# Performance work log

Measured on AMD Instinct MI355X. Metric: run time of the kernel, lower is better.

The kernel has to match this reference:

```python
import jax, jax.numpy as jnp
import numpy as np

DIM = 384
D_STATE = 16


def setup_inputs() -> dict:
    key = jax.random.key(0)
    ks = jax.random.split(key, 8)
    B, C, H, W = 4, DIM, 64, 64
    x = jax.random.normal(ks[0], (B, C, H, W), dtype=jnp.float32)
    P = 2 * DIM + 2 * D_STATE  # proj output width
    W_proj = jax.random.normal(ks[1], (P, DIM), dtype=jnp.float32) * 0.02
    b_proj = jnp.zeros((P,), dtype=jnp.float32)
    # A_log = log(uniform(0,1) + 1e-4) as in torch init
    A_log = jnp.log(jax.random.uniform(ks[2], (DIM, D_STATE), dtype=jnp.float32) + 1e-4)
    D = jnp.ones((DIM,), dtype=jnp.float32)
    dt_bias = jnp.zeros((DIM,), dtype=jnp.float32)
    W_out = jax.random.normal(ks[3], (DIM, DIM), dtype=jnp.float32) * 0.02
    b_out = jnp.zeros((DIM,), dtype=jnp.float32)
    return {"x": x, "W_proj": W_proj, "b_proj": b_proj, "A_log": A_log,
            "D": D, "dt_bias": dt_bias, "W_out": W_out, "b_out": b_out}


def _selective_scan(x_in, delta, A, Bm, Cm, D):
    # x_in, delta: (B, L, dim); Bm, Cm: (B, L, n); A: (dim, n); D: (dim,)
    Bsz, L, dim = x_in.shape
    n = A.shape[1]

    def step(h, inp):
        d_t, x_t, b_t, c_t = inp  # (B,dim),(B,dim),(B,n),(B,n)
        # h: (B, dim, n)
        h = jnp.exp(d_t[..., None] * A) * h + (d_t * x_t)[..., None] * b_t[:, None, :]
        y_t = jnp.einsum('bdn,bn->bd', h, c_t)
        return h, y_t

    h0 = jnp.zeros((Bsz, dim, n), dtype=x_in.dtype)
    xs = (jnp.swapaxes(delta, 0, 1), jnp.swapaxes(x_in, 0, 1),
          jnp.swapaxes(Bm, 0, 1), jnp.swapaxes(Cm, 0, 1))
    _, ys = jax.lax.scan(step, h0, xs)  # ys: (L, B, dim)
    y = jnp.swapaxes(ys, 0, 1)  # (B, L, dim)
    return y + x_in * D


def reference(x, W_proj, b_proj, A_log, D, dt_bias, W_out, b_out):
    B, C, H, W = x.shape
    L = H * W
    seq = x.reshape(B, C, L).transpose(0, 2, 1)  # (B, L, C)
    proj = seq @ W_proj.T + b_proj  # (B, L, 2*dim + 2*n)
    x_in = proj[..., :DIM]
    delta = proj[..., DIM:2 * DIM]
    Bm = proj[..., 2 * DIM:2 * DIM + D_STATE]
    Cm = proj[..., 2 * DIM + D_STATE:]
    A = -jnp.exp(A_log)  # (dim, n)
    delta = jax.nn.softplus(delta + dt_bias)  # delta_bias + delta_softplus
    y = _selective_scan(x_in, delta, A, Bm, Cm, D)  # (B, L, dim)
    out = y @ W_out.T + b_out  # (B, L, dim)
    return out.transpose(0, 2, 1).reshape(B, C, H, W)
```

## Files before the change

kernel.cpp:

```cpp
#include <hip/hip_runtime.h>
#include <cstdint>
#include <cstddef>

#define DIMC 384
#define DST  16
#define LLEN 4096
#define NB   4
#define PDIM 800
#define NCH  64
#define CL   64
#define KDIM 384

typedef __attribute__((ext_vector_type(8))) short bf16x8;
typedef __attribute__((ext_vector_type(4))) float f32x4;

#define GLOAD16(g, l) __builtin_amdgcn_global_load_lds( \
    (const __attribute__((address_space(1))) uint32_t*)(g), \
    (__attribute__((address_space(3))) uint32_t*)(l), 16, 0, 0)

__device__ __forceinline__ float softplus_f(float v) {
    if (v > 20.f) return v;
    return logf(1.f + __expf(v));
}

__device__ __forceinline__ ushort f2bf(float x) {
    uint32_t u = __float_as_uint(x);
    uint32_t r = (u + 0x7FFFu + ((u >> 16) & 1u)) >> 16;
    return (ushort)r;
}

__global__ __launch_bounds__(256)
void cast_bf(const float* __restrict__ in, ushort* __restrict__ out,
             int n_src, int n_tot)
{
    int i = (blockIdx.x * 256 + threadIdx.x) * 4;
    if (i >= n_tot) return;
    if (i < n_src) {
        float4 v = *(const float4*)(in + i);
        ushort4 s; s.x = f2bf(v.x); s.y = f2bf(v.y); s.z = f2bf(v.z); s.w = f2bf(v.w);
        *(ushort4*)(out + i) = s;
    } else {
        ushort4 s; s.x = 0; s.y = 0; s.z = 0; s.w = 0;
        *(ushort4*)(out + i) = s;
    }
}

__global__ __launch_bounds__(256)
void transpose_cast(const float* __restrict__ in, ushort* __restrict__ out)
{
    __shared__ float t[64][65];
    const int tid = threadIdx.x;
    const int b  = blockIdx.z;
    const int c0 = blockIdx.y * 64;
    const int l0 = blockIdx.x * 64;
    const float* ip = in + ((size_t)b * DIMC + c0) * LLEN + l0;
    #pragma unroll
    for (int r = 0; r < 4; ++r) {
        int cl = (tid >> 4) + r * 16;
        int l4 = (tid & 15) * 4;
        float4 v = *(const float4*)(ip + (size_t)cl * LLEN + l4);
        t[cl][l4 + 0] = v.x; t[cl][l4 + 1] = v.y;
        t[cl][l4 + 2] = v.z; t[cl][l4 + 3] = v.w;
    }
    __syncthreads();
    ushort* op = out + ((size_t)b * LLEN + l0) * DIMC + c0;
    #pragma unroll
    for (int r = 0; r < 4; ++r) {
        int ll = (tid >> 4) + r * 16;
        int c4 = (tid & 15) * 4;
        ushort4 s;
        s.x = f2bf(t[c4 + 0][ll]); s.y = f2bf(t[c4 + 1][ll]);
        s.z = f2bf(t[c4 + 2][ll]); s.w = f2bf(t[c4 + 3][ll]);
        *(ushort4*)(op + (size_t)ll * DIMC + c4) = s;
    }
}

template<int EPI>
__global__ __launch_bounds__(256)
void mfma_gemm(const ushort* __restrict__ Abf, const ushort* __restrict__ Wbf,
               const float* __restrict__ bias, const float* __restrict__ dt_bias,
               float* __restrict__ o_x, float* __restrict__ o_dt,
               float* __restrict__ o_Bm, float* __restrict__ o_Cm,
               float* __restrict__ o_out)
{
    __shared__ ushort Alds[128 * 32];
    __shared__ ushort Blds[64 * 32];

    const int tid = threadIdx.x;
    const int m0  = blockIdx.x * 128;
    const int n0  = blockIdx.y * 64;
    const int w   = tid >> 6;
    const int ln  = tid & 63;
    const int wm  = w * 32;
    const int fr  = ln & 15;
    const int fg  = ln >> 4;

    const int srow = tid >> 2;
    const int sg   = tid & 3;

    const ushort* Ag = Abf + (size_t)m0 * KDIM;
    const ushort* Bg = Wbf + (size_t)n0 * KDIM;

    f32x4 acc[2][4];
    #pragma unroll
    for (int i = 0; i < 2; ++i)
        #pragma unroll
        for (int j = 0; j < 4; ++j)
            acc[i][j] = (f32x4){0.f, 0.f, 0.f, 0.f};

    for (int k0 = 0; k0 < KDIM; k0 += 32) {
        if (k0) __syncthreads();
        {
            int a0 = sg ^ ((srow >> 1) & 3);
            GLOAD16(Ag + (size_t)srow * KDIM + k0 + a0 * 8, &Alds[tid * 8]);
            int r1 = srow + 64;
            int a1 = sg ^ ((r1 >> 1) & 3);
            GLOAD16(Ag + (size_t)r1 * KDIM + k0 + a1 * 8, &Alds[2048 + tid * 8]);
            GLOAD16(Bg + (size_t)srow * KDIM + k0 + a0 * 8, &Blds[tid * 8]);
        }
        __syncthreads();
        bf16x8 af[2], bfv[4];
        #pragma unroll
        for (int i = 0; i < 2; ++i) {
            int r = wm + i * 16 + fr;
            af[i] = *(const bf16x8*)&Alds[r * 32 + ((fg ^ ((r >> 1) & 3)) << 3)];
        }
        #pragma unroll
        for (int j = 0; j < 4; ++j) {
            int r = j * 16 + fr;
            bfv[j] = *(const bf16x8*)&Blds[r * 32 + ((fg ^ ((r >> 1) & 3)) << 3)];
        }
        #pragma unroll
        for (int i = 0; i < 2; ++i)
            #pragma unroll
            for (int j = 0; j < 4; ++j)
                acc[i][j] = __builtin_amdgcn_mfma_f32_16x16x32_bf16(af[i], bfv[j], acc[i][j], 0, 0, 0);
    }

    const int b   = m0 / LLEN;
    const int ml0 = m0 - b * LLEN;
    #pragma unroll
    for (int j = 0; j < 4; ++j) {
        const int n = n0 + j * 16 + fr;
        #pragma unroll
        for (int i = 0; i < 2; ++i) {
            const int l = ml0 + wm + i * 16 + fg * 4;
            f32x4 v = acc[i][j];
            if (EPI == 0) {
                if (n < DIMC) {
                    const float bb = bias[n];
                    float4 st; st.x = v[0] + bb; st.y = v[1] + bb; st.z = v[2] + bb; st.w = v[3] + bb;
                    *(float4*)(o_x + ((size_t)b * DIMC + n) * LLEN + l) = st;
                } else if (n < 2 * DIMC) {
                    const int d = n - DIMC;
                    const float bb = bias[n] + dt_bias[d];
                    float4 st;
                    st.x = softplus_f(v[0] + bb); st.y = softplus_f(v[1] + bb);
                    st.z = softplus_f(v[2] + bb); st.w = softplus_f(v[3] + bb);
                    *(float4*)(o_dt + ((size_t)b * DIMC + d) * LLEN + l) = st;
                } else if (n < 2 * DIMC + DST) {
                    const int s = n - 2 * DIMC;
                    const float bb = bias[n];
                    #pragma unroll
                    for (int r = 0; r < 4; ++r)
                        o_Bm[((size_t)b * LLEN + l + r) * DST + s] = v[r] + bb;
                } else if (n < PDIM) {
                    const int s = n - 2 * DIMC - DST;
                    const float bb = bias[n];
                    #pragma unroll
                    for (int r = 0; r < 4; ++r)
                        o_Cm[((size_t)b * LLEN + l + r) * DST + s] = v[r] + bb;
                }
            } else {
                const float bb = bias[n];
                float4 st; st.x = v[0] + bb; st.y = v[1] + bb; st.z = v[2] + bb; st.w = v[3] + bb;
                *(float4*)(o_out + ((size_t)b * DIMC + n) * LLEN + l) = st;
            }
        }
    }
}

__global__ __launch_bounds__(256)
void scan_part1(const float* __restrict__ dt_t, const float* __restrict__ x_t,
                const float* __restrict__ Bm, const float* __restrict__ A_log,
                float* __restrict__ Pc, float* __restrict__ Qc)
{
    const int tid = threadIdx.x;
    const int n   = tid & 15;
    const int g   = blockIdx.x * 16 + (tid >> 4);
    const int bd  = g >> 6;
    const int chk = g & (NCH - 1);
    const int b   = bd / DIMC;
    const int d   = bd - b * DIMC;

    const float Aval = -__expf(A_log[d * DST + n]);
    const float* dtp = dt_t + (size_t)bd * LLEN + chk * CL;
    const float* xp  = x_t  + (size_t)bd * LLEN + chk * CL;
    const float* Bp  = Bm + ((size_t)b * LLEN + chk * CL) * DST + n;

    float P = 1.f, q = 0.f;
    for (int t0 = 0; t0 < CL; t0 += 4) {
        float4 dt4 = *(const float4*)(dtp + t0);
        float4 x4  = *(const float4*)(xp + t0);
        float bv[4];
        #pragma unroll
        for (int j = 0; j < 4; ++j) bv[j] = Bp[(size_t)(t0 + j) * DST];
        float dts[4] = {dt4.x, dt4.y, dt4.z, dt4.w};
        float xs[4]  = {x4.x, x4.y, x4.z, x4.w};
        #pragma unroll
        for (int j = 0; j < 4; ++j) {
            float a = __expf(dts[j] * Aval);
            P *= a;
            q = fmaf(a, q, dts[j] * xs[j] * bv[j]);
        }
    }
    Pc[(size_t)g * DST + n] = P;
    Qc[(size_t)g * DST + n] = q;
}

__global__ __launch_bounds__(256)
void scan_carry(const float* __restrict__ Pc, const float* __restrict__ Qc,
                float* __restrict__ Hin)
{
    const int idx = blockIdx.x * 256 + threadIdx.x;
    const int bd  = idx >> 4;
    const int n   = idx & 15;
    float h = 0.f;
    for (int chk = 0; chk < NCH; ++chk) {
        size_t o = ((size_t)bd * NCH + chk) * DST + n;
        Hin[o] = h;
        h = fmaf(Pc[o], h, Qc[o]);
    }
}

__global__ __launch_bounds__(256)
void scan_part3(const float* __restrict__ dt_t, const float* __restrict__ x_t,
                const float* __restrict__ Bm, const float* __restrict__ Cm,
                const float* __restrict__ A_log, const float* __restrict__ Dv,
                const float* __restrict__ Hin, float* __restrict__ y_t)
{
    const int tid = threadIdx.x;
    const int n   = tid & 15;
    const int g   = blockIdx.x * 16 + (tid >> 4);
    const int bd  = g >> 6;
    const int chk = g & (NCH - 1);
    const int b   = bd / DIMC;
    const int d   = bd - b * DIMC;

    const float Aval = -__expf(A_log[d * DST + n]);
    const float Dd   = Dv[d];
    const float* dtp = dt_t + (size_t)bd * LLEN + chk * CL;
    const float* xp  = x_t  + (size_t)bd * LLEN + chk * CL;
    const float* Bp  = Bm + ((size_t)b * LLEN + chk * CL) * DST + n;
    const float* Cp  = Cm + ((size_t)b * LLEN + chk * CL) * DST + n;
    float*       yp  = y_t + (size_t)bd * LLEN + chk * CL;

    float h = Hin[(size_t)g * DST + n];
    for (int t0 = 0; t0 < CL; t0 += 4) {
        float4 dt4 = *(const float4*)(dtp + t0);
        float4 x4  = *(const float4*)(xp + t0);
        float bv[4], cv[4];
        #pragma unroll
        for (int j = 0; j < 4; ++j) {
            bv[j] = Bp[(size_t)(t0 + j) * DST];
            cv[j] = Cp[(size_t)(t0 + j) * DST];
        }
        float dts[4] = {dt4.x, dt4.y, dt4.z, dt4.w};
        float xs[4]  = {x4.x, x4.y, x4.z, x4.w};
        float ys[4];
        #pragma unroll
        for (int j = 0; j < 4; ++j) {
            float a = __expf(dts[j] * Aval);
            h = fmaf(a, h, dts[j] * xs[j] * bv[j]);
            float p = h * cv[j];
            p += __shfl_xor(p, 1);
            p += __shfl_xor(p, 2);
            p += __shfl_xor(p, 4);
            p += __shfl_xor(p, 8);
            ys[j] = fmaf(xs[j], Dd, p);
        }
        if (n == 0) {
            float4 st; st.x = ys[0]; st.y = ys[1]; st.z = ys[2]; st.w = ys[3];
            *(float4*)(yp + t0) = st;
        }
    }
}

extern "C" void kernel_launch(void* const* d_in, const int* in_sizes, int n_in,
                              void* d_out, int out_size, void* d_ws, size_t ws_size,
                              hipStream_t stream)
{
    const float* x      = (const float*)d_in[0];
    const float* W_proj = (const float*)d_in[1];
    const float* b_proj = (const float*)d_in[2];
    const float* A_log  = (const float*)d_in[3];
    const float* Dv     = (const float*)d_in[4];
    const float* dt_b   = (const float*)d_in[5];
    const float* W_out  = (const float*)d_in[6];
    const float* b_out  = (const float*)d_in[7];
    float* out = (float*)d_out;
    float* ws  = (float*)d_ws;

    const size_t szBD = (size_t)NB * DIMC * LLEN;
    const size_t szBC = (size_t)NB * LLEN * DST;
    const size_t szPQ = (size_t)NB * DIMC * NCH * DST;
    float* x_t  = ws;
    float* dt_t = x_t + szBD;
    float* Bmw  = dt_t + szBD;
    float* Cmw  = Bmw + szBC;
    float* y_t  = Cmw + szBC;
    float* Pc   = y_t + szBD;
    float* Qc   = Pc + szPQ;
    float* Hin  = Qc + szPQ;
    ushort* x_bfT = (ushort*)(Hin + szPQ);
    ushort* y_bfT = x_bfT + szBD;
    ushort* Wp_bf = y_bfT + szBD;
    ushort* Wo_bf = Wp_bf + (size_t)832 * KDIM;

    cast_bf<<<(832 * KDIM) / 1024, 256, 0, stream>>>(W_proj, Wp_bf,
                                                     PDIM * KDIM, 832 * KDIM);
    cast_bf<<<(DIMC * KDIM) / 1024, 256, 0, stream>>>(W_out, Wo_bf,
                                                      DIMC * KDIM, DIMC * KDIM);
    dim3 tg(LLEN / 64, DIMC / 64, NB);
    transpose_cast<<<tg, 256, 0, stream>>>(x, x_bfT);

    dim3 g1((NB * LLEN) / 128, (PDIM + 63) / 64);
    mfma_gemm<0><<<g1, 256, 0, stream>>>(x_bfT, Wp_bf, b_proj, dt_b,
                                         x_t, dt_t, Bmw, Cmw, nullptr);

    const int ngroups = NB * DIMC * NCH;
    scan_part1<<<ngroups / 16, 256, 0, stream>>>(dt_t, x_t, Bmw, A_log, Pc, Qc);
    scan_carry<<<(NB * DIMC * DST) / 256, 256, 0, stream>>>(Pc, Qc, Hin);
    scan_part3<<<ngroups / 16, 256, 0, stream>>>(dt_t, x_t, Bmw, Cmw,
                                                 A_log, Dv, Hin, y_t);

    transpose_cast<<<tg, 256, 0, stream>>>(y_t, y_bfT);

    dim3 g2((NB * LLEN) / 128, DIMC / 64);
    mfma_gemm<1><<<g2, 256, 0, stream>>>(y_bfT, Wo_bf, b_out, nullptr,
                                         nullptr, nullptr, nullptr, nullptr,
                                         out);
}
```

Measured before the change: 248.7 us.

## Restructure chunked scan to thread-per-channel and fuse bf16 transpose into scan output

The scan kernels now give each thread one (batch, channel) with all 16 state lanes held in registers, instead of one lane per thread. B and C for the chunk are staged in shared memory, which removes the per-step shuffle reduction. scan_part3 writes its output directly as transposed bf16, so the separate transpose_cast pass and the fp32 y buffer are gone. The chunk length is halved to 32 and the number of chunks doubled, which keeps enough blocks in flight (512 blocks of 384 threads) at the cost of heavier register use and a longer serial carry pass.

```diff
diff --git a/kernel.cpp b/kernel.cpp
--- a/kernel.cpp
+++ b/kernel.cpp
@@ -7,8 +7,8 @@
 #define LLEN 4096
 #define NB   4
 #define PDIM 800
-#define NCH  64
-#define CL   64
+#define NCH  128
+#define CL   32
 #define KDIM 384
 
 typedef __attribute__((ext_vector_type(8))) short bf16x8;
@@ -180,42 +180,60 @@
     }
 }
 
-__global__ __launch_bounds__(256)
+__global__ __launch_bounds__(384)
 void scan_part1(const float* __restrict__ dt_t, const float* __restrict__ x_t,
                 const float* __restrict__ Bm, const float* __restrict__ A_log,
                 float* __restrict__ Pc, float* __restrict__ Qc)
 {
-    const int tid = threadIdx.x;
-    const int n   = tid & 15;
-    const int g   = blockIdx.x * 16 + (tid >> 4);
-    const int bd  = g >> 6;
-    const int chk = g & (NCH - 1);
-    const int b   = bd / DIMC;
-    const int d   = bd - b * DIMC;
-
-    const float Aval = -__expf(A_log[d * DST + n]);
-    const float* dtp = dt_t + (size_t)bd * LLEN + chk * CL;
-    const float* xp  = x_t  + (size_t)bd * LLEN + chk * CL;
-    const float* Bp  = Bm + ((size_t)b * LLEN + chk * CL) * DST + n;
-
-    float P = 1.f, q = 0.f;
+    __shared__ float Bs[CL][DST];
+    const int d   = threadIdx.x;
+    const int b   = blockIdx.x >> 7;
+    const int chk = blockIdx.x & (NCH - 1);
+    const int l0  = chk * CL;
+
+    if (d < (CL * DST) / 4)
+        ((float4*)&Bs[0][0])[d] =
+            ((const float4*)(Bm + ((size_t)b * LLEN + l0) * DST))[d];
+
+    float Av[DST];
+    #pragma unroll
+    for (int r = 0; r < 4; ++r) {
+        float4 v = *(const float4*)(A_log + d * DST + r * 4);
+        Av[r*4+0] = -__expf(v.x); Av[r*4+1] = -__expf(v.y);
+        Av[r*4+2] = -__expf(v.z); Av[r*4+3] = -__expf(v.w);
+    }
+    __syncthreads();
+
+    const float* dtp = dt_t + ((size_t)b * DIMC + d) * LLEN + l0;
+    const float* xp  = x_t  + ((size_t)b * DIMC + d) * LLEN + l0;
+
+    float P[DST], q[DST];
+    #pragma unroll
+    for (int n = 0; n < DST; ++n) { P[n] = 1.f; q[n] = 0.f; }
+
     for (int t0 = 0; t0 < CL; t0 += 4) {
         float4 dt4 = *(const float4*)(dtp + t0);
         float4 x4  = *(const float4*)(xp + t0);
-        float bv[4];
-        #pragma unroll
-        for (int j = 0; j < 4; ++j) bv[j] = Bp[(size_t)(t0 + j) * DST];
         float dts[4] = {dt4.x, dt4.y, dt4.z, dt4.w};
         float xs[4]  = {x4.x, x4.y, x4.z, x4.w};
         #pragma unroll
         for (int j = 0; j < 4; ++j) {
-            float a = __expf(dts[j] * Aval);
-            P *= a;
-            q = fmaf(a, q, dts[j] * xs[j] * bv[j]);
-        }
-    }
-    Pc[(size_t)g * DST + n] = P;
-    Qc[(size_t)g * DST + n] = q;
+            const float dt  = dts[j];
+            const float dtx = dt * xs[j];
+            #pragma unroll
+            for (int n = 0; n < DST; ++n) {
+                float a = __expf(dt * Av[n]);
+                P[n] *= a;
+                q[n] = fmaf(a, q[n], dtx * Bs[t0 + j][n]);
+            }
+        }
+    }
+    const size_t o = (((size_t)b * NCH + chk) * DIMC + d) * DST;
+    #pragma unroll
+    for (int r = 0; r < 4; ++r) {
+        *(float4*)(Pc + o + r * 4) = *(float4*)&P[r * 4];
+        *(float4*)(Qc + o + r * 4) = *(float4*)&q[r * 4];
+    }
 }
 
 __global__ __launch_bounds__(256)
@@ -225,63 +243,74 @@
     const int idx = blockIdx.x * 256 + threadIdx.x;
     const int bd  = idx >> 4;
     const int n   = idx & 15;
+    const int b   = bd / DIMC;
+    const int d   = bd - b * DIMC;
     float h = 0.f;
     for (int chk = 0; chk < NCH; ++chk) {
-        size_t o = ((size_t)bd * NCH + chk) * DST + n;
+        const size_t o = (((size_t)b * NCH + chk) * DIMC + d) * DST + n;
         Hin[o] = h;
         h = fmaf(Pc[o], h, Qc[o]);
     }
 }
 
-__global__ __launch_bounds__(256)
+__global__ __launch_bounds__(384)
 void scan_part3(const float* __restrict__ dt_t, const float* __restrict__ x_t,
                 const float* __restrict__ Bm, const float* __restrict__ Cm,
                 const float* __restrict__ A_log, const float* __restrict__ Dv,
-                const float* __restrict__ Hin, float* __restrict__ y_t)
-{
-    const int tid = threadIdx.x;
-    const int n   = tid & 15;
-    const int g   = blockIdx.x * 16 + (tid >> 4);
-    const int bd  = g >> 6;
-    const int chk = g & (NCH - 1);
-    const int b   = bd / DIMC;
-    const int d   = bd - b * DIMC;
-
-    const float Aval = -__expf(A_log[d * DST + n]);
-    const float Dd   = Dv[d];
-    const float* dtp = dt_t + (size_t)bd * LLEN + chk * CL;
-    const float* xp  = x_t  + (size_t)bd * LLEN + chk * CL;
-    const float* Bp  = Bm + ((size_t)b * LLEN + chk * CL) * DST + n;
-    const float* Cp  = Cm + ((size_t)b * LLEN + chk * CL) * DST + n;
-    float*       yp  = y_t + (size_t)bd * LLEN + chk * CL;
-
-    float h = Hin[(size_t)g * DST + n];
+                const float* __restrict__ Hin, ushort* __restrict__ y_bfT)
+{
+    __shared__ float Bs[CL][DST];
+    __shared__ float Cs[CL][DST];
+    const int d   = threadIdx.x;
+    const int b   = blockIdx.x >> 7;
+    const int chk = blockIdx.x & (NCH - 1);
+    const int l0  = chk * CL;
+
+    if (d < 128)
+        ((float4*)&Bs[0][0])[d] =
+            ((const float4*)(Bm + ((size_t)b * LLEN + l0) * DST))[d];
+    else if (d < 256)
+        ((float4*)&Cs[0][0])[d - 128] =
+            ((const float4*)(Cm + ((size_t)b * LLEN + l0) * DST))[d - 128];
+
+    float Av[DST];
+    #pragma unroll
+    for (int r = 0; r < 4; ++r) {
+        float4 v = *(const float4*)(A_log + d * DST + r * 4);
+        Av[r*4+0] = -__expf(v.x); Av[r*4+1] = -__expf(v.y);
+        Av[r*4+2] = -__expf(v.z); Av[r*4+3] = -__expf(v.w);
+    }
+    const float Dd = Dv[d];
+    __syncthreads();
+
+    float h[DST];
+    const size_t ho = (((size_t)b * NCH + chk) * DIMC + d) * DST;
+    #pragma unroll
+    for (int r = 0; r < 4; ++r)
+        *(float4*)&h[r * 4] = *(const float4*)(Hin + ho + r * 4);
+
+    const float* dtp = dt_t + ((size_t)b * DIMC + d) * LLEN + l0;
+    const float* xp  = x_t  + ((size_t)b * DIMC + d) * LLEN + l0;
+    ushort* yp = y_bfT + ((size_t)b * LLEN + l0) * DIMC + d;
+
     for (int t0 = 0; t0 < CL; t0 += 4) {
         float4 dt4 = *(const float4*)(dtp + t0);
         float4 x4  = *(const float4*)(xp + t0);
-        float bv[4], cv[4];
-        #pragma unroll
-        for (int j = 0; j < 4; ++j) {
-            bv[j] = Bp[(size_t)(t0 + j) * DST];
-            cv[j] = Cp[(size_t)(t0 + j) * DST];
-        }
         float dts[4] = {dt4.x, dt4.y, dt4.z, dt4.w};
         float xs[4]  = {x4.x, x4.y, x4.z, x4.w};
-        float ys[4];
         #pragma unroll
         for (int j = 0; j < 4; ++j) {
-            float a = __expf(dts[j] * Aval);
-            h = fmaf(a, h, dts[j] * xs[j] * bv[j]);
-            float p = h * cv[j];
-            p += __shfl_xor(p, 1);
-            p += __shfl_xor(p, 2);
-            p += __shfl_xor(p, 4);
-            p += __shfl_xor(p, 8);
-            ys[j] = fmaf(xs[j], Dd, p);
-        }
-        if (n == 0) {
-            float4 st; st.x = ys[0]; st.y = ys[1]; st.z = ys[2]; st.w = ys[3];
-            *(float4*)(yp + t0) = st;
+            const float dt  = dts[j];
+            const float xx  = xs[j];
+            const float dtx = dt * xx;
+            float yv = Dd * xx;
+            #pragma unroll
+            for (int n = 0; n < DST; ++n) {
+                float a = __expf(dt * Av[n]);
+                h[n] = fmaf(a, h[n], dtx * Bs[t0 + j][n]);
+                yv = fmaf(h[n], Cs[t0 + j][n], yv);
+            }
+            yp[(size_t)(t0 + j) * DIMC] = f2bf(yv);
         }
     }
 }
@@ -303,13 +332,12 @@
 
     const size_t szBD = (size_t)NB * DIMC * LLEN;
     const size_t szBC = (size_t)NB * LLEN * DST;
-    const size_t szPQ = (size_t)NB * DIMC * NCH * DST;
+    const size_t szPQ = (size_t)NB * NCH * DIMC * DST;
     float* x_t  = ws;
     float* dt_t = x_t + szBD;
     float* Bmw  = dt_t + szBD;
     float* Cmw  = Bmw + szBC;
-    float* y_t  = Cmw + szBC;
-    float* Pc   = y_t + szBD;
+    float* Pc   = Cmw + szBC;
     float* Qc   = Pc + szPQ;
     float* Hin  = Qc + szPQ;
     ushort* x_bfT = (ushort*)(Hin + szPQ);
@@ -328,13 +356,10 @@
     mfma_gemm<0><<<g1, 256, 0, stream>>>(x_bfT, Wp_bf, b_proj, dt_b,
                                          x_t, dt_t, Bmw, Cmw, nullptr);
 
-    const int ngroups = NB * DIMC * NCH;
-    scan_part1<<<ngroups / 16, 256, 0, stream>>>(dt_t, x_t, Bmw, A_log, Pc, Qc);
+    scan_part1<<<NB * NCH, 384, 0, stream>>>(dt_t, x_t, Bmw, A_log, Pc, Qc);
     scan_carry<<<(NB * DIMC * DST) / 256, 256, 0, stream>>>(Pc, Qc, Hin);
-    scan_part3<<<ngroups / 16, 256, 0, stream>>>(dt_t, x_t, Bmw, Cmw,
-                                                 A_log, Dv, Hin, y_t);
-
-    transpose_cast<<<tg, 256, 0, stream>>>(y_t, y_bfT);
+    scan_part3<<<NB * NCH, 384, 0, stream>>>(dt_t, x_t, Bmw, Cmw,
+                                             A_log, Dv, Hin, y_bfT);
 
     dim3 g2((NB * LLEN) / 128, DIMC / 64);
     mfma_gemm<1><<<g2, 256, 0, stream>>>(y_bfT, Wo_bf, b_out, nullptr,
```

New measurement: 245.6 us. About the same (-1.3%).
